# Kernel optimization log

Hardware: AMD Instinct MI355X
Metric: run time of the kernel (lower is better)

Reference implementation:

```python
import jax, jax.numpy as jnp
import numpy as np

EMBED = 1024
HEADS = 16
GQA_GROUPS = 2
KV_HEADS = HEADS // GQA_GROUPS  # 8
HEAD_DIM = EMBED // HEADS       # 64
ALIBI_ALPHA = 1.0
START_I = 0
N, S = 2, 2048


def setup_inputs() -> dict:
    key = jax.random.key(0)
    ks = jax.random.split(key, 6)
    x = jax.random.normal(ks[0], (N, S, EMBED), dtype=jnp.float32)
    sc = 1.0 / np.sqrt(EMBED)
    Wq = jax.random.normal(ks[1], (HEADS * HEAD_DIM, EMBED), dtype=jnp.float32) * sc
    Wk = jax.random.normal(ks[2], (KV_HEADS * HEAD_DIM, EMBED), dtype=jnp.float32) * sc
    Wv = jax.random.normal(ks[3], (KV_HEADS * HEAD_DIM, EMBED), dtype=jnp.float32) * sc
    Wo = jax.random.normal(ks[4], (EMBED, HEADS * HEAD_DIM), dtype=jnp.float32) * sc
    bo = jax.random.normal(ks[5], (EMBED,), dtype=jnp.float32) * 0.01
    return {"x": x, "Wq": Wq, "Wk": Wk, "Wv": Wv, "Wo": Wo, "bo": bo}


def _alibi_bias(q_len, k_len):
    # slopes[i] = 2**(-alpha*(i+start)) for i in 1..heads  -> shape (1,H,1,1)
    i = jnp.arange(1, HEADS + 1, dtype=jnp.float32)
    slopes = jnp.exp2(-ALIBI_ALPHA * (i + START_I)).reshape(1, HEADS, 1, 1)
    t_q = jnp.arange(q_len, dtype=jnp.float32)
    t_k = jnp.arange(k_len, dtype=jnp.float32)
    dist = jnp.abs(t_q[:, None] - t_k[None, :])  # (Q,K), symmetric (non-causal ALiBi)
    return -dist[None, None] * slopes            # (1,H,Q,K)


def reference(x, Wq, Wk, Wv, Wo, bo):
    n, s, _ = x.shape
    q = (x @ Wq.T).reshape(n, s, HEADS, HEAD_DIM)      # nqhd
    k = (x @ Wk.T).reshape(n, s, KV_HEADS, HEAD_DIM)   # nkhd (kv heads)
    v = (x @ Wv.T).reshape(n, s, KV_HEADS, HEAD_DIM)
    # GQA: repeat_interleave kv heads along head dim
    k = jnp.repeat(k, GQA_GROUPS, axis=2)
    v = jnp.repeat(v, GQA_GROUPS, axis=2)
    energy = jnp.einsum("nqhd,nkhd->nhqk", q, k)
    energy = energy + _alibi_bias(s, s)
    # NOTE: original divides (energy + bias) by sqrt(head_dim) inside softmax
    attn = jax.nn.softmax(energy / jnp.sqrt(jnp.float32(HEAD_DIM)), axis=-1)
    out = jnp.einsum("nhqk,nkhd->nqhd", attn, v).reshape(n, s, HEADS * HEAD_DIM)
    return out @ Wo.T + bo
```

## Files before the change

kernel.cpp:

```cpp
#include <hip/hip_runtime.h>

typedef _Float16 f16;
typedef f16 f16x8 __attribute__((ext_vector_type(8)));
typedef f16 f16x4 __attribute__((ext_vector_type(4)));
typedef float f32x4 __attribute__((ext_vector_type(4)));
typedef float f32x16 __attribute__((ext_vector_type(16)));
typedef unsigned uint4v __attribute__((ext_vector_type(4)));

#define GLL(g, l) __builtin_amdgcn_global_load_lds((const __attribute__((address_space(1))) void*)(g), (__attribute__((address_space(3))) void*)(l), 16, 0, 0)

__global__ __launch_bounds__(256) void cvt_all(
    const float* __restrict__ x, const float* __restrict__ wq, const float* __restrict__ wk,
    const float* __restrict__ wv, const float* __restrict__ wo,
    f16* __restrict__ xh, f16* __restrict__ wqh, f16* __restrict__ wkh,
    f16* __restrict__ wvh, f16* __restrict__ woh)
{
  int i = blockIdx.x * 256 + threadIdx.x;
  const float4* src; f16x4* dst; int off;
  if (i < 1048576)      { src = (const float4*)x;  dst = (f16x4*)xh;  off = i; }
  else if (i < 1310720) { src = (const float4*)wq; dst = (f16x4*)wqh; off = i - 1048576; }
  else if (i < 1441792) { src = (const float4*)wk; dst = (f16x4*)wkh; off = i - 1310720; }
  else if (i < 1572864) { src = (const float4*)wv; dst = (f16x4*)wvh; off = i - 1441792; }
  else                  { src = (const float4*)wo; dst = (f16x4*)woh; off = i - 1572864; }
  float4 v = src[off];
  f16x4 hv; hv[0] = (f16)v.x; hv[1] = (f16)v.y; hv[2] = (f16)v.z; hv[3] = (f16)v.w;
  dst[off] = hv;
}

template<int MODE>
__global__ __launch_bounds__(256) void gemm_k(
    const f16* __restrict__ A, const f16* __restrict__ B0, const f16* __restrict__ B1,
    const f16* __restrict__ B2,
    f16* __restrict__ Qb, f16* __restrict__ Kb, f16* __restrict__ VTb,
    const float* __restrict__ bo, float* __restrict__ Co)
{
  __shared__ __align__(16) f16 Ah[2][4096];
  __shared__ __align__(16) f16 Bh[2][4096];
  const int tid = threadIdx.x;
  const int bm = blockIdx.x & 31, bn = blockIdx.x >> 5;
  const f16* Bp;
  if (MODE == 0) {
    if (bn < 8)       Bp = B0 + (size_t)bn * 131072;
    else if (bn < 12) Bp = B1 + (size_t)(bn - 8) * 131072;
    else              Bp = B2 + (size_t)(bn - 12) * 131072;
  } else {
    Bp = B0 + (size_t)bn * 131072;
  }
  const f16* Ap = A + (size_t)bm * 131072;

  const int w = tid >> 6, lane = tid & 63, lr = lane & 15, lg = lane >> 4;
  const int wr = w >> 1, wc = w & 1;

  auto stage = [&](int b, int kt) {
#pragma unroll
    for (int i = 0; i < 2; ++i) {
      int o = tid * 16 + i * 4096;
      int row = o >> 6, colb = o & 63;
      GLL((const char*)Ap + (size_t)row * 2048 + kt * 64 + colb, (char*)&Ah[b][0] + o);
      GLL((const char*)Bp + (size_t)row * 2048 + kt * 64 + colb, (char*)&Bh[b][0] + o);
    }
  };

  f32x4 acc[4][4] = {};

  stage(0, 0);
  for (int kt = 0; kt < 32; ++kt) {
    const int cur = kt & 1;
    __syncthreads();
    if (kt < 31) stage(cur ^ 1, kt + 1);
    f16x8 af[4], bf[4];
#pragma unroll
    for (int mi = 0; mi < 4; ++mi)
      af[mi] = *(const f16x8*)((const char*)&Ah[cur][0] + (wr * 64 + mi * 16 + lr) * 64 + lg * 16);
#pragma unroll
    for (int ni = 0; ni < 4; ++ni)
      bf[ni] = *(const f16x8*)((const char*)&Bh[cur][0] + (wc * 64 + ni * 16 + lr) * 64 + lg * 16);
#pragma unroll
    for (int mi = 0; mi < 4; ++mi)
#pragma unroll
      for (int ni = 0; ni < 4; ++ni)
        acc[mi][ni] = __builtin_amdgcn_mfma_f32_16x16x32_f16(af[mi], bf[ni], acc[mi][ni], 0, 0, 0);
    __syncthreads();
  }

#pragma unroll
  for (int mi = 0; mi < 4; ++mi) {
#pragma unroll
    for (int ni = 0; ni < 4; ++ni) {
      const int ncol = bn * 128 + wc * 64 + ni * 16 + lr;
#pragma unroll
      for (int j = 0; j < 4; ++j) {
        const int m = bm * 128 + wr * 64 + mi * 16 + lg * 4 + j;
        const float v = acc[mi][ni][j];
        if (MODE == 0) {
          const int nb = m >> 11, s = m & 2047;
          if (ncol < 1024) {
            const int hh = ncol >> 6, d = ncol & 63;
            Qb[(((size_t)(nb * 16 + hh)) * 2048 + s) * 64 + d] = (f16)v;
          } else if (ncol < 1536) {
            const int kh = (ncol - 1024) >> 6, d = ncol & 63;
            Kb[(((size_t)(nb * 8 + kh)) * 2048 + s) * 64 + d] = (f16)v;
          } else {
            const int vh = (ncol - 1536) >> 6, d = ncol & 63;
            VTb[(((size_t)(nb * 8 + vh)) * 64 + d) * 2048 + s] = (f16)v;
          }
        } else {
          Co[(size_t)m * 1024 + ncol] = v + bo[ncol];
        }
      }
    }
  }
}

__global__ __launch_bounds__(512, 4) void attn_k(
    const f16* __restrict__ Qb, const f16* __restrict__ Kb, const f16* __restrict__ VTb,
    f16* __restrict__ Ob)
{
  __shared__ __align__(16) char SMEM[65536];

  const int tid = threadIdx.x, w = tid >> 6, l = tid & 63;
  const int lq = l & 31, hi = l >> 5;
  const int half = w >> 2, g = w & 3;
  const int qt = blockIdx.x, nh = blockIdx.y;
  const int n = nh >> 4, h = nh & 15, kvh = h >> 1;
  const int qb = qt * 128;
  const int qhat = qb + g * 32 + lq;

  const f16* Qp = Qb + ((size_t)(n * 16 + h) * 2048 + qhat) * 64;
  f16x8 qf[4];
#pragma unroll
  for (int cd = 0; cd < 4; ++cd)
    qf[cd] = *(const f16x8*)(Qp + cd * 16 + hi * 8);

  const char* Kg = (const char*)(Kb + (size_t)(n * 8 + kvh) * 2048 * 64);
  const char* Vg = (const char*)(VTb + (size_t)(n * 8 + kvh) * 64 * 2048);

  const int t256 = tid & 255;
  const int s0 = t256 * 16, s1 = s0 + 4096;
  const int r0 = s0 >> 7, c0 = ((s0 >> 4) & 7) ^ (r0 & 7);
  const int r1 = s1 >> 7, c1 = ((s1 >> 4) & 7) ^ (r1 & 7);
  char* KB0 = SMEM + half * 32768;

  auto stageK = [&](int buf, int tb) {
    char* d = KB0 + buf * 16384;
    GLL(Kg + (size_t)(tb * 64 + r0) * 128 + c0 * 16, d + s0);
    GLL(Kg + (size_t)(tb * 64 + r1) * 128 + c1 * 16, d + s1);
  };
  auto stageV = [&](int buf, int tb) {
    char* d = KB0 + buf * 16384 + 8192;
    GLL(Vg + (size_t)r0 * 4096 + tb * 128 + c0 * 16, d + s0);
    GLL(Vg + (size_t)r1 * 4096 + tb * 128 + c1 * 16, d + s1);
  };

  f32x16 oacc[2] = {};
  float p[2][16];
  float m_r = -1e30f, l_r = 0.f;
  const float C1 = 0.18033688011112042f;
  const float slt = exp2f(-(float)(h + 1)) * C1;
  const float qpos = (float)qhat;

  stageK(0, half * 16); stageV(0, half * 16);

  for (int t = 0; t < 16; ++t) {
    const int cur = t & 1;
    const int tb = half * 16 + t;
    __syncthreads();
    if (t < 15) { stageK(cur ^ 1, tb + 1); stageV(cur ^ 1, tb + 1); }
    const char* Kl = KB0 + cur * 16384;
    const char* Vl = Kl + 8192;

#pragma unroll
    for (int kt = 0; kt < 2; ++kt) {
      f32x16 c = {};
#pragma unroll
      for (int cd = 0; cd < 4; ++cd) {
        const int row = kt * 32 + lq;
        f16x8 kf = *(const f16x8*)(Kl + row * 128 + (((2 * cd + hi) ^ (row & 7)) * 16));
        c = __builtin_amdgcn_mfma_f32_32x32x16_f16(kf, qf[cd], c, 0, 0, 0);
      }
      const float kb0 = (float)(tb * 64 + kt * 32 + 4 * hi);
#pragma unroll
      for (int r = 0; r < 16; ++r) {
        float kpos = kb0 + (float)((r & 3) + 8 * (r >> 2));
        p[kt][r] = c[r] * C1 - fabsf(qpos - kpos) * slt;
      }
    }
    float pmax = p[0][0];
#pragma unroll
    for (int kt = 0; kt < 2; ++kt)
#pragma unroll
      for (int r = 0; r < 16; ++r) pmax = fmaxf(pmax, p[kt][r]);
    pmax = fmaxf(pmax, __shfl_xor(pmax, 32));

    if (!__all(pmax - m_r <= 8.0f)) {
      float mn = fmaxf(m_r, pmax);
      float sc = __builtin_amdgcn_exp2f(m_r - mn);
      m_r = mn; l_r *= sc;
#pragma unroll
      for (int dt = 0; dt < 2; ++dt)
#pragma unroll
        for (int r = 0; r < 16; ++r) oacc[dt][r] *= sc;
    }
    float ps = 0.f;
#pragma unroll
    for (int kt = 0; kt < 2; ++kt)
#pragma unroll
      for (int r = 0; r < 16; ++r) {
        float e = __builtin_amdgcn_exp2f(p[kt][r] - m_r);
        p[kt][r] = e; ps += e;
      }
    ps += __shfl_xor(ps, 32);
    l_r += ps;

    f16x8 pf[4];
#pragma unroll
    for (int c2 = 0; c2 < 4; ++c2) {
      const int T = c2 >> 1, e = c2 & 1;
      unsigned w0 = __builtin_bit_cast(unsigned, __builtin_amdgcn_cvt_pkrtz(p[T][8 * e + 0], p[T][8 * e + 1]));
      unsigned w2 = __builtin_bit_cast(unsigned, __builtin_amdgcn_cvt_pkrtz(p[T][8 * e + 4], p[T][8 * e + 5]));
      unsigned w1 = __builtin_bit_cast(unsigned, __builtin_amdgcn_cvt_pkrtz(p[T][8 * e + 2], p[T][8 * e + 3]));
      unsigned w3 = __builtin_bit_cast(unsigned, __builtin_amdgcn_cvt_pkrtz(p[T][8 * e + 6], p[T][8 * e + 7]));
      asm volatile("v_permlane32_swap_b32 %0, %1" : "+v"(w0), "+v"(w2));
      asm volatile("v_permlane32_swap_b32 %0, %1" : "+v"(w1), "+v"(w3));
      uint4v pu; pu.x = w0; pu.y = w1; pu.z = w2; pu.w = w3;
      pf[c2] = __builtin_bit_cast(f16x8, pu);
    }

#pragma unroll
    for (int dt = 0; dt < 2; ++dt) {
#pragma unroll
      for (int ck = 0; ck < 4; ++ck) {
        const int row = dt * 32 + lq;
        f16x8 vf = *(const f16x8*)(Vl + row * 128 + (((2 * ck + hi) ^ (row & 7)) * 16));
        oacc[dt] = __builtin_amdgcn_mfma_f32_32x32x16_f16(vf, pf[ck], oacc[dt], 0, 0, 0);
      }
    }
  }

  float* Xo = (float*)SMEM;
  float* Xm = (float*)(SMEM + 33792);
  float* Xl = (float*)(SMEM + 34304);
  f16* Ot = (f16*)SMEM;

  __syncthreads();
  if (half) {
#pragma unroll
    for (int dt = 0; dt < 2; ++dt)
#pragma unroll
      for (int r = 0; r < 16; ++r) {
        const int d = dt * 32 + (r & 3) + 8 * (r >> 2) + 4 * hi;
        Xo[(g * 32 + lq) * 66 + d] = oacc[dt][r];
      }
    if (!hi) { Xm[g * 32 + lq] = m_r; Xl[g * 32 + lq] = l_r; }
  }
  __syncthreads();
  float fin[2][16];
  if (!half) {
    const float m1 = Xm[g * 32 + lq], l1 = Xl[g * 32 + lq];
    const float mm = fmaxf(m_r, m1);
    const float a0 = __builtin_amdgcn_exp2f(m_r - mm);
    const float a1 = __builtin_amdgcn_exp2f(m1 - mm);
    const float linv = 1.0f / (l_r * a0 + l1 * a1);
#pragma unroll
    for (int dt = 0; dt < 2; ++dt)
#pragma unroll
      for (int r = 0; r < 16; ++r) {
        const int d = dt * 32 + (r & 3) + 8 * (r >> 2) + 4 * hi;
        fin[dt][r] = (oacc[dt][r] * a0 + Xo[(g * 32 + lq) * 66 + d] * a1) * linv;
      }
  }
  __syncthreads();
  if (!half) {
#pragma unroll
    for (int dt = 0; dt < 2; ++dt)
#pragma unroll
      for (int r = 0; r < 16; ++r) {
        const int d = dt * 32 + (r & 3) + 8 * (r >> 2) + 4 * hi;
        Ot[(g * 32 + lq) * 72 + d] = (f16)fin[dt][r];
      }
  }
  __syncthreads();
  {
    const int q = tid >> 2, seg = tid & 3;
    const f16* src = &Ot[q * 72 + seg * 16];
    f16* dst = Ob + (size_t)(n * 2048 + qb + q) * 1024 + h * 64 + seg * 16;
    *(f16x8*)(dst) = *(const f16x8*)(src);
    *(f16x8*)(dst + 8) = *(const f16x8*)(src + 8);
  }
}

extern "C" void kernel_launch(void* const* d_in, const int* in_sizes, int n_in,
                              void* d_out, int out_size, void* d_ws, size_t ws_size,
                              hipStream_t stream) {
  const float* x  = (const float*)d_in[0];
  const float* Wq = (const float*)d_in[1];
  const float* Wk = (const float*)d_in[2];
  const float* Wv = (const float*)d_in[3];
  const float* Wo = (const float*)d_in[4];
  const float* bo = (const float*)d_in[5];

  char* ws = (char*)d_ws;
  f16* xh  = (f16*)(ws);
  f16* wqh = (f16*)(ws + 8388608);
  f16* wkh = (f16*)(ws + 10485760);
  f16* wvh = (f16*)(ws + 11534336);
  f16* woh = (f16*)(ws + 12582912);
  f16* Qb  = (f16*)(ws + 14680064);
  f16* Kb  = (f16*)(ws + 23068672);
  f16* VTb = (f16*)(ws + 27262976);
  f16* Ob  = (f16*)(ws + 31457280);

  cvt_all<<<7168, 256, 0, stream>>>(x, Wq, Wk, Wv, Wo, xh, wqh, wkh, wvh, woh);
  gemm_k<0><<<512, 256, 0, stream>>>(xh, wqh, wkh, wvh, Qb, Kb, VTb, nullptr, nullptr);
  attn_k<<<dim3(16, 32), 512, 0, stream>>>(Qb, Kb, VTb, Ob);
  gemm_k<1><<<256, 256, 0, stream>>>(Ob, woh, nullptr, nullptr, nullptr, nullptr, nullptr, bo, (float*)d_out);
}
```

Before: 133.4 us.

## Compute V transposed via separate GEMM, fold softmax scale into Q, MFMA row sums

Measured after the change: 144.8 us. +8.5%, slower.

```diff
diff --git a/kernel.cpp b/kernel.cpp
--- a/kernel.cpp
+++ b/kernel.cpp
@@ -30,8 +30,7 @@
 template<int MODE>
 __global__ __launch_bounds__(256) void gemm_k(
     const f16* __restrict__ A, const f16* __restrict__ B0, const f16* __restrict__ B1,
-    const f16* __restrict__ B2,
-    f16* __restrict__ Qb, f16* __restrict__ Kb, f16* __restrict__ VTb,
+    f16* __restrict__ Qb, f16* __restrict__ Kb,
     const float* __restrict__ bo, float* __restrict__ Co)
 {
   __shared__ __align__(16) f16 Ah[2][4096];
@@ -40,9 +39,8 @@
   const int bm = blockIdx.x & 31, bn = blockIdx.x >> 5;
   const f16* Bp;
   if (MODE == 0) {
-    if (bn < 8)       Bp = B0 + (size_t)bn * 131072;
-    else if (bn < 12) Bp = B1 + (size_t)(bn - 8) * 131072;
-    else              Bp = B2 + (size_t)(bn - 12) * 131072;
+    if (bn < 8)  Bp = B0 + (size_t)bn * 131072;
+    else         Bp = B1 + (size_t)(bn - 8) * 131072;
   } else {
     Bp = B0 + (size_t)bn * 131072;
   }
@@ -83,6 +81,7 @@
     __syncthreads();
   }
 
+  const float C1 = 0.18033688011112042f;
 #pragma unroll
   for (int mi = 0; mi < 4; ++mi) {
 #pragma unroll
@@ -96,13 +95,10 @@
           const int nb = m >> 11, s = m & 2047;
           if (ncol < 1024) {
             const int hh = ncol >> 6, d = ncol & 63;
-            Qb[(((size_t)(nb * 16 + hh)) * 2048 + s) * 64 + d] = (f16)v;
-          } else if (ncol < 1536) {
+            Qb[(((size_t)(nb * 16 + hh)) * 2048 + s) * 64 + d] = (f16)(v * C1);
+          } else {
             const int kh = (ncol - 1024) >> 6, d = ncol & 63;
             Kb[(((size_t)(nb * 8 + kh)) * 2048 + s) * 64 + d] = (f16)v;
-          } else {
-            const int vh = (ncol - 1536) >> 6, d = ncol & 63;
-            VTb[(((size_t)(nb * 8 + vh)) * 64 + d) * 2048 + s] = (f16)v;
           }
         } else {
           Co[(size_t)m * 1024 + ncol] = v + bo[ncol];
@@ -112,7 +108,69 @@
   }
 }
 
-__global__ __launch_bounds__(512, 4) void attn_k(
+__global__ __launch_bounds__(256) void gemm_vt(
+    const f16* __restrict__ A,
+    const f16* __restrict__ B,
+    f16* __restrict__ C)
+{
+  __shared__ __align__(16) f16 Ah[2][2048];
+  __shared__ __align__(16) f16 Bh[2][4096];
+  const int tid = threadIdx.x;
+  const int bm = blockIdx.x & 7, bn = blockIdx.x >> 3;
+  const f16* Ap = A + (size_t)bm * 65536;
+  const f16* Bp = B + (size_t)bn * 131072;
+  const int w = tid >> 6, lane = tid & 63, lr = lane & 15, lg = lane >> 4;
+  const int wr = w >> 1, wc = w & 1;
+
+  auto stage = [&](int b, int kt) {
+    {
+      int o = tid * 16;
+      int row = o >> 6, colb = o & 63;
+      GLL((const char*)Ap + (size_t)row * 2048 + kt * 64 + colb, (char*)&Ah[b][0] + o);
+    }
+#pragma unroll
+    for (int i = 0; i < 2; ++i) {
+      int o = tid * 16 + i * 4096;
+      int row = o >> 6, colb = o & 63;
+      GLL((const char*)Bp + (size_t)row * 2048 + kt * 64 + colb, (char*)&Bh[b][0] + o);
+    }
+  };
+
+  f32x4 acc[2][4] = {};
+  stage(0, 0);
+  for (int kt = 0; kt < 32; ++kt) {
+    const int cur = kt & 1;
+    __syncthreads();
+    if (kt < 31) stage(cur ^ 1, kt + 1);
+    f16x8 af[2], bf[4];
+#pragma unroll
+    for (int mi = 0; mi < 2; ++mi)
+      af[mi] = *(const f16x8*)((const char*)&Ah[cur][0] + (wr * 32 + mi * 16 + lr) * 64 + lg * 16);
+#pragma unroll
+    for (int ni = 0; ni < 4; ++ni)
+      bf[ni] = *(const f16x8*)((const char*)&Bh[cur][0] + (wc * 64 + ni * 16 + lr) * 64 + lg * 16);
+#pragma unroll
+    for (int mi = 0; mi < 2; ++mi)
+#pragma unroll
+      for (int ni = 0; ni < 4; ++ni)
+        acc[mi][ni] = __builtin_amdgcn_mfma_f32_16x16x32_f16(af[mi], bf[ni], acc[mi][ni], 0, 0, 0);
+    __syncthreads();
+  }
+
+#pragma unroll
+  for (int mi = 0; mi < 2; ++mi)
+#pragma unroll
+    for (int ni = 0; ni < 4; ++ni) {
+      const int ncol = bn * 128 + wc * 64 + ni * 16 + lr;
+#pragma unroll
+      for (int j = 0; j < 4; ++j) {
+        const int m = bm * 64 + wr * 32 + mi * 16 + lg * 4 + j;
+        C[(size_t)m * 4096 + ncol] = (f16)acc[mi][ni][j];
+      }
+    }
+}
+
+__global__ __launch_bounds__(512, 2) void attn_k(
     const f16* __restrict__ Qb, const f16* __restrict__ Kb, const f16* __restrict__ VTb,
     f16* __restrict__ Ob)
 {
@@ -133,7 +191,7 @@
     qf[cd] = *(const f16x8*)(Qp + cd * 16 + hi * 8);
 
   const char* Kg = (const char*)(Kb + (size_t)(n * 8 + kvh) * 2048 * 64);
-  const char* Vg = (const char*)(VTb + (size_t)(n * 8 + kvh) * 64 * 2048);
+  const char* Vg = (const char*)(VTb + (size_t)kvh * 64 * 4096 + (size_t)n * 2048);
 
   const int t256 = tid & 255;
   const int s0 = t256 * 16, s1 = s0 + 4096;
@@ -148,16 +206,21 @@
   };
   auto stageV = [&](int buf, int tb) {
     char* d = KB0 + buf * 16384 + 8192;
-    GLL(Vg + (size_t)r0 * 4096 + tb * 128 + c0 * 16, d + s0);
-    GLL(Vg + (size_t)r1 * 4096 + tb * 128 + c1 * 16, d + s1);
+    GLL(Vg + (size_t)r0 * 8192 + tb * 128 + c0 * 16, d + s0);
+    GLL(Vg + (size_t)r1 * 8192 + tb * 128 + c1 * 16, d + s1);
   };
 
   f32x16 oacc[2] = {};
+  f32x16 lacc = {};
   float p[2][16];
-  float m_r = -1e30f, l_r = 0.f;
+  float m_r = -1e30f;
   const float C1 = 0.18033688011112042f;
   const float slt = exp2f(-(float)(h + 1)) * C1;
   const float qpos = (float)qhat;
+
+  f16x8 ones;
+#pragma unroll
+  for (int i = 0; i < 8; ++i) ones[i] = (f16)1.0f;
 
   stageK(0, half * 16); stageV(0, half * 16);
 
@@ -182,9 +245,10 @@
 #pragma unroll
       for (int r = 0; r < 16; ++r) {
         float kpos = kb0 + (float)((r & 3) + 8 * (r >> 2));
-        p[kt][r] = c[r] * C1 - fabsf(qpos - kpos) * slt;
-      }
-    }
+        p[kt][r] = fmaf(-fabsf(qpos - kpos), slt, c[r]);
+      }
+    }
+
     float pmax = p[0][0];
 #pragma unroll
     for (int kt = 0; kt < 2; ++kt)
@@ -195,22 +259,19 @@
     if (!__all(pmax - m_r <= 8.0f)) {
       float mn = fmaxf(m_r, pmax);
       float sc = __builtin_amdgcn_exp2f(m_r - mn);
-      m_r = mn; l_r *= sc;
+      m_r = mn;
 #pragma unroll
       for (int dt = 0; dt < 2; ++dt)
 #pragma unroll
         for (int r = 0; r < 16; ++r) oacc[dt][r] *= sc;
-    }
-    float ps = 0.f;
+#pragma unroll
+      for (int r = 0; r < 16; ++r) lacc[r] *= sc;
+    }
 #pragma unroll
     for (int kt = 0; kt < 2; ++kt)
 #pragma unroll
-      for (int r = 0; r < 16; ++r) {
-        float e = __builtin_amdgcn_exp2f(p[kt][r] - m_r);
-        p[kt][r] = e; ps += e;
-      }
-    ps += __shfl_xor(ps, 32);
-    l_r += ps;
+      for (int r = 0; r < 16; ++r)
+        p[kt][r] = __builtin_amdgcn_exp2f(p[kt][r] - m_r);
 
     f16x8 pf[4];
 #pragma unroll
@@ -235,7 +296,12 @@
         oacc[dt] = __builtin_amdgcn_mfma_f32_32x32x16_f16(vf, pf[ck], oacc[dt], 0, 0, 0);
       }
     }
-  }
+#pragma unroll
+    for (int ck = 0; ck < 4; ++ck)
+      lacc = __builtin_amdgcn_mfma_f32_32x32x16_f16(ones, pf[ck], lacc, 0, 0, 0);
+  }
+
+  const float l_r = lacc[0];
 
   float* Xo = (float*)SMEM;
   float* Xm = (float*)(SMEM + 33792);
@@ -311,7 +377,8 @@
   f16* Ob  = (f16*)(ws + 31457280);
 
   cvt_all<<<7168, 256, 0, stream>>>(x, Wq, Wk, Wv, Wo, xh, wqh, wkh, wvh, woh);
-  gemm_k<0><<<512, 256, 0, stream>>>(xh, wqh, wkh, wvh, Qb, Kb, VTb, nullptr, nullptr);
+  gemm_k<0><<<384, 256, 0, stream>>>(xh, wqh, wkh, Qb, Kb, nullptr, nullptr);
+  gemm_vt<<<256, 256, 0, stream>>>(wvh, xh, VTb);
   attn_k<<<dim3(16, 32), 512, 0, stream>>>(Qb, Kb, VTb, Ob);
-  gemm_k<1><<<256, 256, 0, stream>>>(Ob, woh, nullptr, nullptr, nullptr, nullptr, nullptr, bo, (float*)d_out);
-}
+  gemm_k<1><<<256, 256, 0, stream>>>(Ob, woh, nullptr, nullptr, nullptr, bo, (float*)d_out);
+}
```
